# Kernel optimization log

Measured on AMD Instinct MI355X. Metric: run time of the kernel, lower is better.

The kernel has to match this reference:

```python
import jax, jax.numpy as jnp
from jax import lax
import numpy as np

N_MACRO, HIDDEN, N_LAYERS, N_REGIMES, N_ASSETS = 16, 256, 2, 3, 32
VIX_THRESHOLD, DEFENSIVE_ALLOC, EPSILON = 30.0, 0.4, 1e-8
N_EQ = 24  # equities = assets[:24], defensive = assets[24:]
N_DEF = N_ASSETS - N_EQ
LN_EPS = 1e-5


def setup_inputs() -> dict:
    key = jax.random.key(0)
    ks = jax.random.split(key, 16)
    B, S = 128, 1024
    inp = {
        'macro_features': jax.random.normal(ks[0], (B, S, N_MACRO), jnp.float32),
        'vix_values': jax.random.uniform(ks[1], (B,), jnp.float32) * 60.0,  # some above threshold
    }
    k = 1.0 / np.sqrt(HIDDEN)
    def u(kk, shape):
        return jax.random.uniform(kk, shape, jnp.float32, -k, k)
    # layer 0
    inp['lstm_Wih0'] = u(ks[2], (4 * HIDDEN, N_MACRO))
    inp['lstm_Whh0'] = u(ks[3], (4 * HIDDEN, HIDDEN))
    inp['lstm_bih0'] = u(ks[4], (4 * HIDDEN,))
    inp['lstm_bhh0'] = u(ks[5], (4 * HIDDEN,))
    # layer 1
    inp['lstm_Wih1'] = u(ks[6], (4 * HIDDEN, HIDDEN))
    inp['lstm_Whh1'] = u(ks[7], (4 * HIDDEN, HIDDEN))
    inp['lstm_bih1'] = u(ks[8], (4 * HIDDEN,))
    inp['lstm_bhh1'] = u(ks[9], (4 * HIDDEN,))
    inp['ln_gamma'] = jnp.ones((HIDDEN,), jnp.float32)
    inp['ln_beta'] = jnp.zeros((HIDDEN,), jnp.float32)
    inp['logits_W'] = u(ks[10], (N_REGIMES, HIDDEN))
    inp['logits_b'] = u(ks[11], (N_REGIMES,))
    inp['risk_budgets'] = jax.random.normal(ks[12], (N_REGIMES, N_ASSETS), jnp.float32) * 0.01
    return inp


def _lstm_layer(x, Wih, Whh, bih, bhh):
    # x: [B,S,I] -> h sequence [B,S,H]
    B = x.shape[0]
    H = Whh.shape[1]
    pre = jnp.einsum('bsi,gi->bsg', x, Wih) + bih + bhh  # [B,S,4H]
    def step(carry, p):
        h, c = carry
        g = p + h @ Whh.T
        i, f, gg, o = jnp.split(g, 4, axis=-1)
        c = jax.nn.sigmoid(f) * c + jax.nn.sigmoid(i) * jnp.tanh(gg)
        h = jax.nn.sigmoid(o) * jnp.tanh(c)
        return (h, c), h
    init = (jnp.zeros((B, H), x.dtype), jnp.zeros((B, H), x.dtype))
    _, hs = lax.scan(step, init, jnp.swapaxes(pre, 0, 1))
    return jnp.swapaxes(hs, 0, 1)


def _vix_override(beta, vix_mask):
    # vectorized version of the per-sample override loop
    eq, df = beta[:, :N_EQ], beta[:, N_EQ:]
    cur_def = df.sum(-1)
    shortfall = DEFENSIVE_ALLOC - cur_def
    eq_total = eq.sum(-1)
    ratio = jnp.minimum(shortfall / jnp.maximum(eq_total, EPSILON), 0.8)
    apply = vix_mask & (shortfall > 0) & (eq_total > EPSILON)
    new_eq = eq * (1.0 - ratio)[:, None]
    new_df = df + (shortfall / N_DEF)[:, None]
    b2 = jnp.concatenate([new_eq, new_df], axis=-1)
    b = jnp.where(apply[:, None], b2, beta)
    b_norm = b / (b.sum(-1, keepdims=True) + EPSILON)
    return jnp.where(vix_mask[:, None], b_norm, beta)


def reference(macro_features, vix_values,
              lstm_Wih0, lstm_Whh0, lstm_bih0, lstm_bhh0,
              lstm_Wih1, lstm_Whh1, lstm_bih1, lstm_bhh1,
              ln_gamma, ln_beta, logits_W, logits_b, risk_budgets):
    h1 = _lstm_layer(macro_features, lstm_Wih0, lstm_Whh0, lstm_bih0, lstm_bhh0)
    h2 = _lstm_layer(h1, lstm_Wih1, lstm_Whh1, lstm_bih1, lstm_bhh1)
    h_last = h2[:, -1, :]  # [B,H]
    mu = h_last.mean(-1, keepdims=True)
    var = ((h_last - mu) ** 2).mean(-1, keepdims=True)
    h_norm = (h_last - mu) / jnp.sqrt(var + LN_EPS) * ln_gamma + ln_beta
    regime_probs = jax.nn.softmax(h_norm @ logits_W.T + logits_b, axis=-1)  # [B,K]
    budgets = jax.nn.softmax(risk_budgets, axis=-1)  # [K,P]
    beta = jnp.einsum('bk,kp->bp', regime_probs, budgets)
    vix_mask = vix_values >= VIX_THRESHOLD
    beta = _vix_override(beta, vix_mask)
    return beta, regime_probs
```

## Files before the change

kernel.cpp:

```cpp
#include <hip/hip_runtime.h>

#define B_  128
#define S_  1024
#define H_  256
#define NM_ 16
#define NEG_INF_TGT (-0x7FFFFFFF)

typedef short bf16x8 __attribute__((ext_vector_type(8)));
typedef float f32x4  __attribute__((ext_vector_type(4)));

__device__ __forceinline__ short f2bf(float f) {
    unsigned u = __builtin_bit_cast(unsigned, f);
    unsigned r = (u + 0x7FFFu + ((u >> 16) & 1u)) >> 16;
    return (short)r;
}
__device__ __forceinline__ bf16x8 zero8() {
    bf16x8 v;
    #pragma unroll
    for (int j = 0; j < 8; ++j) v[j] = 0;
    return v;
}
__device__ __forceinline__ float sigf(float x)  { return 1.0f / (1.0f + __expf(-x)); }
__device__ __forceinline__ float tanh_(float x) { return 1.0f - 2.0f / (1.0f + __expf(2.0f * x)); }
__device__ __forceinline__ void vm_drain() {
    asm volatile("s_waitcnt vmcnt(0)" ::: "memory");
}

__device__ __forceinline__ int cload_int(const int* p) {
    int r;
    asm volatile("global_load_dword %0, %1, off sc0 sc1\n\ts_waitcnt vmcnt(0)"
                 : "=v"(r) : "v"(p) : "memory");
    return r;
}
__device__ __forceinline__ void cstore_int(int* p, int v) {
    asm volatile("global_store_dword %0, %1, off sc0 sc1" :: "v"(p), "v"(v) : "memory");
}
__device__ __forceinline__ void cstore_short(short* p, int v) {
    asm volatile("global_store_short %0, %1, off sc0 sc1" :: "v"(p), "v"(v) : "memory");
}
__device__ __forceinline__ void cload8x16(const short* p, bf16x8* d) {
    int4 a0, a1, a2, a3, a4, a5, a6, a7;
    asm volatile(
        "global_load_dwordx4 %0, %8, off sc0 sc1\n\t"
        "global_load_dwordx4 %1, %8, off offset:64 sc0 sc1\n\t"
        "global_load_dwordx4 %2, %8, off offset:128 sc0 sc1\n\t"
        "global_load_dwordx4 %3, %8, off offset:192 sc0 sc1\n\t"
        "global_load_dwordx4 %4, %8, off offset:256 sc0 sc1\n\t"
        "global_load_dwordx4 %5, %8, off offset:320 sc0 sc1\n\t"
        "global_load_dwordx4 %6, %8, off offset:384 sc0 sc1\n\t"
        "global_load_dwordx4 %7, %8, off offset:448 sc0 sc1\n\t"
        "s_waitcnt vmcnt(0)"
        : "=&v"(a0), "=&v"(a1), "=&v"(a2), "=&v"(a3),
          "=&v"(a4), "=&v"(a5), "=&v"(a6), "=&v"(a7)
        : "v"(p) : "memory");
    d[0] = __builtin_bit_cast(bf16x8, a0); d[1] = __builtin_bit_cast(bf16x8, a1);
    d[2] = __builtin_bit_cast(bf16x8, a2); d[3] = __builtin_bit_cast(bf16x8, a3);
    d[4] = __builtin_bit_cast(bf16x8, a4); d[5] = __builtin_bit_cast(bf16x8, a5);
    d[6] = __builtin_bit_cast(bf16x8, a6); d[7] = __builtin_bit_cast(bf16x8, a7);
}

__device__ __forceinline__ void tag_poll(const int* tagp, int tgt) {
    for (;;) {
        int tv = cload_int(tagp);
        if (__all(tv >= tgt)) break;
    }
}

__device__ void run_l0(const float* __restrict__ x, const float* __restrict__ Wih0,
                       const float* __restrict__ Whh0, const float* __restrict__ bih0,
                       const float* __restrict__ bhh0, short* __restrict__ h1ring,
                       int* __restrict__ tags0, int* __restrict__ tags1, int g, int q)
{
    const int lane = threadIdx.x & 63, wv = threadIdx.x >> 6;
    const int n = lane & 15, quad = lane >> 4;
    const int hu_base = q * 64 + wv * 16;
    bf16x8 wf[4][9];
    float  bias[4];
    #pragma unroll
    for (int G = 0; G < 4; ++G) {
        int col = G * 256 + hu_base + n;
        bias[G] = bih0[col] + bhh0[col];
        #pragma unroll
        for (int kt = 0; kt < 8; ++kt) {
            const float* p = Whh0 + (long)col * H_ + kt * 32 + quad * 8;
            bf16x8 v;
            #pragma unroll
            for (int j = 0; j < 8; ++j) v[j] = f2bf(p[j]);
            wf[G][kt] = v;
        }
        bf16x8 v = zero8();
        if (quad < 2) {
            const float* p = Wih0 + (long)col * NM_ + quad * 8;
            #pragma unroll
            for (int j = 0; j < 8; ++j) v[j] = f2bf(p[j]);
        }
        wf[G][8] = v;
    }
    const int bRow = g * 16 + n;
    const int* tagp = (lane < 16) ? (tags0 + (g * 16 + lane) * 16)
                    : (lane < 32) ? (tags1 + (g * 16 + lane - 16) * 16)
                                  : (tags0 + g * 16 * 16);
    int* mytag = tags0 + (g * 16 + q * 4 + wv) * 16;
    f32x4 c = {0.f, 0.f, 0.f, 0.f};
    for (int t = 0; t < S_; ++t) {
        bf16x8 xfrag = zero8();
        if (quad < 2) {
            const float* p = x + ((long)bRow * S_ + t) * NM_ + quad * 8;
            #pragma unroll
            for (int j = 0; j < 8; ++j) xfrag[j] = f2bf(p[j]);
        }
        const int tgt = (lane < 16) ? t : ((lane < 32) ? (t - 15) : NEG_INF_TGT);
        tag_poll(tagp, tgt);

        bf16x8 af[9];
        if (t > 0) {
            cload8x16(h1ring + ((long)((t - 1) & 15) * B_ + bRow) * H_ + quad * 8, af);
        } else {
            #pragma unroll
            for (int kt = 0; kt < 8; ++kt) af[kt] = zero8();
        }
        af[8] = xfrag;

        f32x4 acc[4];
        #pragma unroll
        for (int G = 0; G < 4; ++G) {
            acc[G][0] = bias[G]; acc[G][1] = bias[G];
            acc[G][2] = bias[G]; acc[G][3] = bias[G];
        }
        #pragma unroll
        for (int kt = 0; kt < 9; ++kt)
            #pragma unroll
            for (int G = 0; G < 4; ++G)
                acc[G] = __builtin_amdgcn_mfma_f32_16x16x32_bf16(af[kt], wf[G][kt], acc[G], 0, 0, 0);
        #pragma unroll
        for (int r = 0; r < 4; ++r) {
            float iv = sigf(acc[0][r]);
            float fv = sigf(acc[1][r]);
            float gv = tanh_(acc[2][r]);
            float ov = sigf(acc[3][r]);
            c[r] = fv * c[r] + iv * gv;
            float hv = ov * tanh_(c[r]);
            int b = g * 16 + quad * 4 + r;
            cstore_short(h1ring + ((long)(t & 15) * B_ + b) * H_ + hu_base + n,
                         (int)(unsigned short)f2bf(hv));
        }
        vm_drain();
        if (lane == 0) cstore_int(mytag, t + 1);
    }
}

__device__ void run_l1(const float* __restrict__ Wih1, const float* __restrict__ Whh1,
                       const float* __restrict__ bih1, const float* __restrict__ bhh1,
                       short* __restrict__ h1ring, short* __restrict__ h2ring,
                       float* __restrict__ hlast,
                       int* __restrict__ tags0, int* __restrict__ tags1, int g, int q)
{
    const int lane = threadIdx.x & 63, wv = threadIdx.x >> 6;
    const int n = lane & 15, quad = lane >> 4;
    const int hu_base = q * 64 + wv * 16;
    bf16x8 wf[4][16];
    float  bias[4];
    #pragma unroll
    for (int G = 0; G < 4; ++G) {
        int col = G * 256 + hu_base + n;
        bias[G] = bih1[col] + bhh1[col];
        #pragma unroll
        for (int kt = 0; kt < 8; ++kt) {
            const float* p = Whh1 + (long)col * H_ + kt * 32 + quad * 8;
            bf16x8 v;
            #pragma unroll
            for (int j = 0; j < 8; ++j) v[j] = f2bf(p[j]);
            wf[G][kt] = v;
        }
        #pragma unroll
        for (int kt = 0; kt < 8; ++kt) {
            const float* p = Wih1 + (long)col * H_ + kt * 32 + quad * 8;
            bf16x8 v;
            #pragma unroll
            for (int j = 0; j < 8; ++j) v[j] = f2bf(p[j]);
            wf[G][8 + kt] = v;
        }
    }
    const int bRow = g * 16 + n;
    const int* tagp = (lane < 16) ? (tags0 + (g * 16 + lane) * 16)
                    : (lane < 32) ? (tags1 + (g * 16 + lane - 16) * 16)
                                  : (tags1 + g * 16 * 16);
    int* mytag = tags1 + (g * 16 + q * 4 + wv) * 16;
    f32x4 c = {0.f, 0.f, 0.f, 0.f};
    for (int t = 0; t < S_; ++t) {
        const int tgt = (lane < 16) ? (t + 1) : ((lane < 32) ? t : NEG_INF_TGT);
        tag_poll(tagp, tgt);

        bf16x8 af[16];
        if (t > 0) {
            cload8x16(h2ring + ((long)((t - 1) & 1) * B_ + bRow) * H_ + quad * 8, af);
        } else {
            #pragma unroll
            for (int kt = 0; kt < 8; ++kt) af[kt] = zero8();
        }
        cload8x16(h1ring + ((long)(t & 15) * B_ + bRow) * H_ + quad * 8, af + 8);

        f32x4 acc[4];
        #pragma unroll
        for (int G = 0; G < 4; ++G) {
            acc[G][0] = bias[G]; acc[G][1] = bias[G];
            acc[G][2] = bias[G]; acc[G][3] = bias[G];
        }
        #pragma unroll
        for (int kt = 0; kt < 16; ++kt)
            #pragma unroll
            for (int G = 0; G < 4; ++G)
                acc[G] = __builtin_amdgcn_mfma_f32_16x16x32_bf16(af[kt], wf[G][kt], acc[G], 0, 0, 0);
        #pragma unroll
        for (int r = 0; r < 4; ++r) {
            float iv = sigf(acc[0][r]);
            float fv = sigf(acc[1][r]);
            float gv = tanh_(acc[2][r]);
            float ov = sigf(acc[3][r]);
            c[r] = fv * c[r] + iv * gv;
            float hv = ov * tanh_(c[r]);
            int b = g * 16 + quad * 4 + r;
            cstore_short(h2ring + ((long)(t & 1) * B_ + b) * H_ + hu_base + n,
                         (int)(unsigned short)f2bf(hv));
            if (t == S_ - 1) hlast[b * H_ + hu_base + n] = hv;
        }
        vm_drain();
        if (lane == 0) cstore_int(mytag, t + 1);
    }
}

__global__ __launch_bounds__(256, 1) void lstm_kernel(
    const float* __restrict__ x,
    const float* __restrict__ Wih0, const float* __restrict__ Whh0,
    const float* __restrict__ bih0, const float* __restrict__ bhh0,
    const float* __restrict__ Wih1, const float* __restrict__ Whh1,
    const float* __restrict__ bih1, const float* __restrict__ bhh1,
    short* __restrict__ h1ring, short* __restrict__ h2ring,
    float* __restrict__ hlast,
    int* __restrict__ tags0, int* __restrict__ tags1)
{
    const int g    = blockIdx.x & 7;
    const int role = blockIdx.x >> 3;
    if (role < 4) run_l0(x, Wih0, Whh0, bih0, bhh0, h1ring, tags0, tags1, g, role);
    else          run_l1(Wih1, Whh1, bih1, bhh1, h1ring, h2ring, hlast, tags0, tags1, g, role - 4);
}

__device__ __forceinline__ float blockSum(float v, float* sbuf) {
    #pragma unroll
    for (int off = 32; off > 0; off >>= 1) v += __shfl_down(v, off, 64);
    __syncthreads();
    if ((threadIdx.x & 63) == 0) sbuf[threadIdx.x >> 6] = v;
    __syncthreads();
    return sbuf[0] + sbuf[1] + sbuf[2] + sbuf[3];
}

__global__ __launch_bounds__(256) void tail_kernel(
    const float* __restrict__ hlast, const float* __restrict__ gamma,
    const float* __restrict__ lnbeta, const float* __restrict__ Wl,
    const float* __restrict__ bl, const float* __restrict__ rb,
    const float* __restrict__ vix, float* __restrict__ out)
{
    __shared__ float sbuf[4];
    __shared__ float pr[3], mxs[3], dens[3];
    __shared__ float bvec[32];
    const int b   = blockIdx.x;
    const int tid = threadIdx.x;

    float v  = hlast[b * H_ + tid];
    float mu = blockSum(v, sbuf) * (1.0f / 256.0f);
    float d  = v - mu;
    float var = blockSum(d * d, sbuf) * (1.0f / 256.0f);
    float hn  = d * rsqrtf(var + 1e-5f) * gamma[tid] + lnbeta[tid];

    float l[3];
    #pragma unroll
    for (int k = 0; k < 3; ++k)
        l[k] = blockSum(hn * Wl[k * H_ + tid], sbuf) + bl[k];

    if (tid == 0) {
        float m  = fmaxf(l[0], fmaxf(l[1], l[2]));
        float e0 = __expf(l[0] - m), e1 = __expf(l[1] - m), e2 = __expf(l[2] - m);
        float dn = e0 + e1 + e2;
        pr[0] = e0 / dn; pr[1] = e1 / dn; pr[2] = e2 / dn;
    }
    if (tid < 3) {
        float m = -1e30f;
        for (int p = 0; p < 32; ++p) m = fmaxf(m, rb[tid * 32 + p]);
        float dn = 0.f;
        for (int p = 0; p < 32; ++p) dn += __expf(rb[tid * 32 + p] - m);
        mxs[tid] = m; dens[tid] = dn;
    }
    __syncthreads();
    if (tid < 32) {
        float bp = 0.f;
        #pragma unroll
        for (int k = 0; k < 3; ++k)
            bp += pr[k] * __expf(rb[k * 32 + tid] - mxs[k]) / dens[k];
        bvec[tid] = bp;
    }
    __syncthreads();
    if (tid == 0) {
        bool  mask = vix[b] >= 30.0f;
        float eq_total = 0.f, cur_def = 0.f;
        for (int p = 0; p < 24; ++p) eq_total += bvec[p];
        for (int p = 24; p < 32; ++p) cur_def += bvec[p];
        float shortfall = 0.4f - cur_def;
        float ratio = fminf(shortfall / fmaxf(eq_total, 1e-8f), 0.8f);
        bool  apply = mask && (shortfall > 0.0f) && (eq_total > 1e-8f);
        float bb[32]; float ssum = 0.f;
        for (int p = 0; p < 32; ++p) {
            float b2 = (p < 24) ? bvec[p] * (1.0f - ratio) : bvec[p] + shortfall * (1.0f / 8.0f);
            float bv = apply ? b2 : bvec[p];
            bb[p] = bv; ssum += bv;
        }
        float inv = 1.0f / (ssum + 1e-8f);
        for (int p = 0; p < 32; ++p)
            out[b * 32 + p] = mask ? bb[p] * inv : bvec[p];
        #pragma unroll
        for (int k = 0; k < 3; ++k)
            out[B_ * 32 + b * 3 + k] = pr[k];
    }
}

extern "C" void kernel_launch(void* const* d_in, const int* in_sizes, int n_in,
                              void* d_out, int out_size, void* d_ws, size_t ws_size,
                              hipStream_t stream)
{
    const float* x    = (const float*)d_in[0];
    const float* vix  = (const float*)d_in[1];
    const float* Wih0 = (const float*)d_in[2];
    const float* Whh0 = (const float*)d_in[3];
    const float* bih0 = (const float*)d_in[4];
    const float* bhh0 = (const float*)d_in[5];
    const float* Wih1 = (const float*)d_in[6];
    const float* Whh1 = (const float*)d_in[7];
    const float* bih1 = (const float*)d_in[8];
    const float* bhh1 = (const float*)d_in[9];
    const float* lng  = (const float*)d_in[10];
    const float* lnb  = (const float*)d_in[11];
    const float* Wl   = (const float*)d_in[12];
    const float* bl   = (const float*)d_in[13];
    const float* rb   = (const float*)d_in[14];
    float* out = (float*)d_out;

    char*  ws     = (char*)d_ws;
    short* h1ring = (short*)ws;
    short* h2ring = (short*)(ws + 1048576);
    float* hlast  = (float*)(ws + 1179648);
    int*   tags0  = (int*)(ws + 1310720);
    int*   tags1  = (int*)(ws + 1318912);

    hipMemsetAsync(ws + 1310720, 0, 16384, stream);
    lstm_kernel<<<64, 256, 0, stream>>>(x, Wih0, Whh0, bih0, bhh0,
                                        Wih1, Whh1, bih1, bhh1,
                                        h1ring, h2ring, hlast, tags0, tags1);
    tail_kernel<<<128, 256, 0, stream>>>(hlast, lng, lnb, Wl, bl, rb, vix, out);
}
```

Measured before the change: 4.822 ms.

## Embed step tags in hidden-state words to replace separate flag polling

Each bf16 hidden value is stored in a 32-bit word with the low 16 bits holding the timestep tag. Consumers poll the data rows directly until every tag matches, so the separate per-wave tag stores, the drain before them, and the dependency polls are removed. Backpressure is handled with a lighter async check on layer-1 progress, and the h2 ring grows from 2 to 4 slots. In exchange the data volume moved per step doubles, and retry loops reload whole rows.

```diff
diff --git a/kernel.cpp b/kernel.cpp
--- a/kernel.cpp
+++ b/kernel.cpp
@@ -4,7 +4,6 @@
 #define S_  1024
 #define H_  256
 #define NM_ 16
-#define NEG_INF_TGT (-0x7FFFFFFF)
 
 typedef short bf16x8 __attribute__((ext_vector_type(8)));
 typedef float f32x4  __attribute__((ext_vector_type(4)));
@@ -32,44 +31,73 @@
                  : "=v"(r) : "v"(p) : "memory");
     return r;
 }
+__device__ __forceinline__ int cload_int_nw(const int* p) {
+    int r;
+    asm volatile("global_load_dword %0, %1, off sc0 sc1" : "=&v"(r) : "v"(p) : "memory");
+    return r;
+}
 __device__ __forceinline__ void cstore_int(int* p, int v) {
     asm volatile("global_store_dword %0, %1, off sc0 sc1" :: "v"(p), "v"(v) : "memory");
 }
-__device__ __forceinline__ void cstore_short(short* p, int v) {
-    asm volatile("global_store_short %0, %1, off sc0 sc1" :: "v"(p), "v"(v) : "memory");
-}
-__device__ __forceinline__ void cload8x16(const short* p, bf16x8* d) {
-    int4 a0, a1, a2, a3, a4, a5, a6, a7;
+__device__ __forceinline__ void cstore_word(unsigned* p, unsigned v) {
+    asm volatile("global_store_dword %0, %1, off sc0 sc1" :: "v"(p), "v"(v) : "memory");
+}
+__device__ __forceinline__ void row_lo_nw(const unsigned* p, int4* d) {
     asm volatile(
         "global_load_dwordx4 %0, %8, off sc0 sc1\n\t"
-        "global_load_dwordx4 %1, %8, off offset:64 sc0 sc1\n\t"
+        "global_load_dwordx4 %1, %8, off offset:16 sc0 sc1\n\t"
         "global_load_dwordx4 %2, %8, off offset:128 sc0 sc1\n\t"
-        "global_load_dwordx4 %3, %8, off offset:192 sc0 sc1\n\t"
+        "global_load_dwordx4 %3, %8, off offset:144 sc0 sc1\n\t"
         "global_load_dwordx4 %4, %8, off offset:256 sc0 sc1\n\t"
-        "global_load_dwordx4 %5, %8, off offset:320 sc0 sc1\n\t"
+        "global_load_dwordx4 %5, %8, off offset:272 sc0 sc1\n\t"
         "global_load_dwordx4 %6, %8, off offset:384 sc0 sc1\n\t"
-        "global_load_dwordx4 %7, %8, off offset:448 sc0 sc1\n\t"
-        "s_waitcnt vmcnt(0)"
-        : "=&v"(a0), "=&v"(a1), "=&v"(a2), "=&v"(a3),
-          "=&v"(a4), "=&v"(a5), "=&v"(a6), "=&v"(a7)
+        "global_load_dwordx4 %7, %8, off offset:400 sc0 sc1"
+        : "=&v"(d[0]), "=&v"(d[1]), "=&v"(d[2]), "=&v"(d[3]),
+          "=&v"(d[4]), "=&v"(d[5]), "=&v"(d[6]), "=&v"(d[7])
         : "v"(p) : "memory");
-    d[0] = __builtin_bit_cast(bf16x8, a0); d[1] = __builtin_bit_cast(bf16x8, a1);
-    d[2] = __builtin_bit_cast(bf16x8, a2); d[3] = __builtin_bit_cast(bf16x8, a3);
-    d[4] = __builtin_bit_cast(bf16x8, a4); d[5] = __builtin_bit_cast(bf16x8, a5);
-    d[6] = __builtin_bit_cast(bf16x8, a6); d[7] = __builtin_bit_cast(bf16x8, a7);
-}
-
-__device__ __forceinline__ void tag_poll(const int* tagp, int tgt) {
-    for (;;) {
-        int tv = cload_int(tagp);
-        if (__all(tv >= tgt)) break;
+}
+__device__ __forceinline__ void row_hi_nw(const unsigned* p, int4* d) {
+    asm volatile(
+        "global_load_dwordx4 %0, %8, off offset:512 sc0 sc1\n\t"
+        "global_load_dwordx4 %1, %8, off offset:528 sc0 sc1\n\t"
+        "global_load_dwordx4 %2, %8, off offset:640 sc0 sc1\n\t"
+        "global_load_dwordx4 %3, %8, off offset:656 sc0 sc1\n\t"
+        "global_load_dwordx4 %4, %8, off offset:768 sc0 sc1\n\t"
+        "global_load_dwordx4 %5, %8, off offset:784 sc0 sc1\n\t"
+        "global_load_dwordx4 %6, %8, off offset:896 sc0 sc1\n\t"
+        "global_load_dwordx4 %7, %8, off offset:912 sc0 sc1"
+        : "=&v"(d[0]), "=&v"(d[1]), "=&v"(d[2]), "=&v"(d[3]),
+          "=&v"(d[4]), "=&v"(d[5]), "=&v"(d[6]), "=&v"(d[7])
+        : "v"(p) : "memory");
+}
+__device__ __forceinline__ unsigned tagmask16(const int4* w, unsigned tgt) {
+    unsigned mm = 0;
+    #pragma unroll
+    for (int i = 0; i < 16; ++i) {
+        mm |= ((unsigned)w[i].x ^ tgt) & 0xFFFFu;
+        mm |= ((unsigned)w[i].y ^ tgt) & 0xFFFFu;
+        mm |= ((unsigned)w[i].z ^ tgt) & 0xFFFFu;
+        mm |= ((unsigned)w[i].w ^ tgt) & 0xFFFFu;
+    }
+    return mm;
+}
+__device__ __forceinline__ void unpack8(const int4* w, bf16x8* af) {
+    #pragma unroll
+    for (int k = 0; k < 8; ++k) {
+        int4 A = w[2 * k], Bv = w[2 * k + 1];
+        int4 r;
+        r.x = (int)(((unsigned)A.x  >> 16) | ((unsigned)A.y  & 0xFFFF0000u));
+        r.y = (int)(((unsigned)A.z  >> 16) | ((unsigned)A.w  & 0xFFFF0000u));
+        r.z = (int)(((unsigned)Bv.x >> 16) | ((unsigned)Bv.y & 0xFFFF0000u));
+        r.w = (int)(((unsigned)Bv.z >> 16) | ((unsigned)Bv.w & 0xFFFF0000u));
+        af[k] = __builtin_bit_cast(bf16x8, r);
     }
 }
 
 __device__ void run_l0(const float* __restrict__ x, const float* __restrict__ Wih0,
                        const float* __restrict__ Whh0, const float* __restrict__ bih0,
-                       const float* __restrict__ bhh0, short* __restrict__ h1ring,
-                       int* __restrict__ tags0, int* __restrict__ tags1, int g, int q)
+                       const float* __restrict__ bhh0, unsigned* __restrict__ h1w,
+                       int* __restrict__ tags1, int g, int q)
 {
     const int lane = threadIdx.x & 63, wv = threadIdx.x >> 6;
     const int n = lane & 15, quad = lane >> 4;
@@ -96,11 +124,9 @@
         }
         wf[G][8] = v;
     }
-    const int bRow = g * 16 + n;
-    const int* tagp = (lane < 16) ? (tags0 + (g * 16 + lane) * 16)
-                    : (lane < 32) ? (tags1 + (g * 16 + lane - 16) * 16)
-                                  : (tags0 + g * 16 * 16);
-    int* mytag = tags0 + (g * 16 + q * 4 + wv) * 16;
+    const int  bRow = g * 16 + n;
+    const bool bplane = (lane >= 16 && lane < 32);
+    const int* tp = tags1 + (g * 16 + ((lane - 16) & 15)) * 16;
     f32x4 c = {0.f, 0.f, 0.f, 0.f};
     for (int t = 0; t < S_; ++t) {
         bf16x8 xfrag = zero8();
@@ -109,17 +135,29 @@
             #pragma unroll
             for (int j = 0; j < 8; ++j) xfrag[j] = f2bf(p[j]);
         }
-        const int tgt = (lane < 16) ? t : ((lane < 32) ? (t - 15) : NEG_INF_TGT);
-        tag_poll(tagp, tgt);
-
         bf16x8 af[9];
         if (t > 0) {
-            cload8x16(h1ring + ((long)((t - 1) & 15) * B_ + bRow) * H_ + quad * 8, af);
+            const unsigned tgt = (unsigned)t & 0xFFFFu;
+            const unsigned* p = h1w + ((long)((t - 1) & 15) * B_ + bRow) * H_ + quad * 8;
+            int4 raw[16];
+            row_lo_nw(p, raw); row_hi_nw(p, raw + 8);
+            vm_drain(); __builtin_amdgcn_sched_barrier(0);
+            for (;;) {
+                unsigned mm = tagmask16(raw, tgt);
+                if (__all(mm == 0)) break;
+                __builtin_amdgcn_s_sleep(1);
+                row_lo_nw(p, raw); row_hi_nw(p, raw + 8);
+                vm_drain(); __builtin_amdgcn_sched_barrier(0);
+            }
+            unpack8(raw, af);
         } else {
             #pragma unroll
             for (int kt = 0; kt < 8; ++kt) af[kt] = zero8();
         }
         af[8] = xfrag;
+
+        int bpv = 0;
+        if (bplane) bpv = cload_int_nw(tp);
 
         f32x4 acc[4];
         #pragma unroll
@@ -132,6 +170,8 @@
             #pragma unroll
             for (int G = 0; G < 4; ++G)
                 acc[G] = __builtin_amdgcn_mfma_f32_16x16x32_bf16(af[kt], wf[G][kt], acc[G], 0, 0, 0);
+
+        unsigned wd[4];
         #pragma unroll
         for (int r = 0; r < 4; ++r) {
             float iv = sigf(acc[0][r]);
@@ -140,20 +180,29 @@
             float ov = sigf(acc[3][r]);
             c[r] = fv * c[r] + iv * gv;
             float hv = ov * tanh_(c[r]);
+            wd[r] = ((unsigned)(unsigned short)f2bf(hv) << 16) | ((unsigned)(t + 1) & 0xFFFFu);
+        }
+        vm_drain(); __builtin_amdgcn_sched_barrier(0);
+        {
+            const int bptgt = t - 15;
+            int ok = bplane ? (bpv >= bptgt) : 1;
+            while (!__all(ok)) {
+                if (bplane) bpv = cload_int(tp);
+                ok = bplane ? (bpv >= bptgt) : 1;
+            }
+        }
+        #pragma unroll
+        for (int r = 0; r < 4; ++r) {
             int b = g * 16 + quad * 4 + r;
-            cstore_short(h1ring + ((long)(t & 15) * B_ + b) * H_ + hu_base + n,
-                         (int)(unsigned short)f2bf(hv));
-        }
-        vm_drain();
-        if (lane == 0) cstore_int(mytag, t + 1);
+            cstore_word(h1w + ((long)(t & 15) * B_ + b) * H_ + hu_base + n, wd[r]);
+        }
     }
 }
 
 __device__ void run_l1(const float* __restrict__ Wih1, const float* __restrict__ Whh1,
                        const float* __restrict__ bih1, const float* __restrict__ bhh1,
-                       short* __restrict__ h1ring, short* __restrict__ h2ring,
-                       float* __restrict__ hlast,
-                       int* __restrict__ tags0, int* __restrict__ tags1, int g, int q)
+                       unsigned* __restrict__ h1w, unsigned* __restrict__ h2w,
+                       float* __restrict__ hlast, int* __restrict__ tags1, int g, int q)
 {
     const int lane = threadIdx.x & 63, wv = threadIdx.x >> 6;
     const int n = lane & 15, quad = lane >> 4;
@@ -181,24 +230,42 @@
             wf[G][8 + kt] = v;
         }
     }
-    const int bRow = g * 16 + n;
-    const int* tagp = (lane < 16) ? (tags0 + (g * 16 + lane) * 16)
-                    : (lane < 32) ? (tags1 + (g * 16 + lane - 16) * 16)
-                                  : (tags1 + g * 16 * 16);
+    const int  bRow = g * 16 + n;
+    const bool bplane = (lane >= 16 && lane < 32);
+    const int* tp = tags1 + (g * 16 + ((lane - 16) & 15)) * 16;
     int* mytag = tags1 + (g * 16 + q * 4 + wv) * 16;
     f32x4 c = {0.f, 0.f, 0.f, 0.f};
     for (int t = 0; t < S_; ++t) {
-        const int tgt = (lane < 16) ? (t + 1) : ((lane < 32) ? t : NEG_INF_TGT);
-        tag_poll(tagp, tgt);
+        const unsigned tgt2 = (unsigned)t & 0xFFFFu;
+        const unsigned tgt1 = (unsigned)(t + 1) & 0xFFFFu;
+        const unsigned* p2 = h2w + ((long)((t - 1) & 3) * B_ + bRow) * H_ + quad * 8;
+        const unsigned* p1 = h1w + ((long)(t & 15) * B_ + bRow) * H_ + quad * 8;
+        int4 raw2[16], raw1[16];
+        if (t > 0) { row_lo_nw(p2, raw2); row_hi_nw(p2, raw2 + 8); }
+        row_lo_nw(p1, raw1); row_hi_nw(p1, raw1 + 8);
+        vm_drain(); __builtin_amdgcn_sched_barrier(0);
+        for (;;) {
+            unsigned mm = tagmask16(raw1, tgt1);
+            if (t > 0) mm |= tagmask16(raw2, tgt2);
+            if (__all(mm == 0)) break;
+            __builtin_amdgcn_s_sleep(1);
+            if (t > 0) { row_lo_nw(p2, raw2); row_hi_nw(p2, raw2 + 8); }
+            row_lo_nw(p1, raw1); row_hi_nw(p1, raw1 + 8);
+            vm_drain(); __builtin_amdgcn_sched_barrier(0);
+        }
+        if (lane == 0) cstore_int(mytag, t + 1);
+
+        int bpv = 0;
+        if (bplane) bpv = cload_int_nw(tp);
 
         bf16x8 af[16];
         if (t > 0) {
-            cload8x16(h2ring + ((long)((t - 1) & 1) * B_ + bRow) * H_ + quad * 8, af);
+            unpack8(raw2, af);
         } else {
             #pragma unroll
             for (int kt = 0; kt < 8; ++kt) af[kt] = zero8();
         }
-        cload8x16(h1ring + ((long)(t & 15) * B_ + bRow) * H_ + quad * 8, af + 8);
+        unpack8(raw1, af + 8);
 
         f32x4 acc[4];
         #pragma unroll
@@ -211,6 +278,8 @@
             #pragma unroll
             for (int G = 0; G < 4; ++G)
                 acc[G] = __builtin_amdgcn_mfma_f32_16x16x32_bf16(af[kt], wf[G][kt], acc[G], 0, 0, 0);
+
+        unsigned wd[4]; float hvout[4];
         #pragma unroll
         for (int r = 0; r < 4; ++r) {
             float iv = sigf(acc[0][r]);
@@ -219,13 +288,24 @@
             float ov = sigf(acc[3][r]);
             c[r] = fv * c[r] + iv * gv;
             float hv = ov * tanh_(c[r]);
+            hvout[r] = hv;
+            wd[r] = ((unsigned)(unsigned short)f2bf(hv) << 16) | ((unsigned)(t + 1) & 0xFFFFu);
+        }
+        vm_drain(); __builtin_amdgcn_sched_barrier(0);
+        {
+            const int bptgt = t - 2;
+            int ok = bplane ? (bpv >= bptgt) : 1;
+            while (!__all(ok)) {
+                if (bplane) bpv = cload_int(tp);
+                ok = bplane ? (bpv >= bptgt) : 1;
+            }
+        }
+        #pragma unroll
+        for (int r = 0; r < 4; ++r) {
             int b = g * 16 + quad * 4 + r;
-            cstore_short(h2ring + ((long)(t & 1) * B_ + b) * H_ + hu_base + n,
-                         (int)(unsigned short)f2bf(hv));
-            if (t == S_ - 1) hlast[b * H_ + hu_base + n] = hv;
-        }
-        vm_drain();
-        if (lane == 0) cstore_int(mytag, t + 1);
+            cstore_word(h2w + ((long)(t & 3) * B_ + b) * H_ + hu_base + n, wd[r]);
+            if (t == S_ - 1) hlast[b * H_ + hu_base + n] = hvout[r];
+        }
     }
 }
 
@@ -235,14 +315,13 @@
     const float* __restrict__ bih0, const float* __restrict__ bhh0,
     const float* __restrict__ Wih1, const float* __restrict__ Whh1,
     const float* __restrict__ bih1, const float* __restrict__ bhh1,
-    short* __restrict__ h1ring, short* __restrict__ h2ring,
-    float* __restrict__ hlast,
-    int* __restrict__ tags0, int* __restrict__ tags1)
+    unsigned* __restrict__ h1w, unsigned* __restrict__ h2w,
+    float* __restrict__ hlast, int* __restrict__ tags1)
 {
     const int g    = blockIdx.x & 7;
     const int role = blockIdx.x >> 3;
-    if (role < 4) run_l0(x, Wih0, Whh0, bih0, bhh0, h1ring, tags0, tags1, g, role);
-    else          run_l1(Wih1, Whh1, bih1, bhh1, h1ring, h2ring, hlast, tags0, tags1, g, role - 4);
+    if (role < 4) run_l0(x, Wih0, Whh0, bih0, bhh0, h1w, tags1, g, role);
+    else          run_l1(Wih1, Whh1, bih1, bhh1, h1w, h2w, hlast, tags1, g, role - 4);
 }
 
 __device__ __forceinline__ float blockSum(float v, float* sbuf) {
@@ -343,16 +422,16 @@
     const float* rb   = (const float*)d_in[14];
     float* out = (float*)d_out;
 
-    char*  ws     = (char*)d_ws;
-    short* h1ring = (short*)ws;
-    short* h2ring = (short*)(ws + 1048576);
-    float* hlast  = (float*)(ws + 1179648);
-    int*   tags0  = (int*)(ws + 1310720);
-    int*   tags1  = (int*)(ws + 1318912);
-
-    hipMemsetAsync(ws + 1310720, 0, 16384, stream);
+    char*     ws    = (char*)d_ws;
+    unsigned* h1w   = (unsigned*)ws;
+    unsigned* h2w   = (unsigned*)(ws + 2097152);
+    float*    hlast = (float*)(ws + 2621440);
+    int*      tags1 = (int*)(ws + 2752512);
+
+    (void)hipMemsetAsync(ws, 0, 2621440, stream);
+    (void)hipMemsetAsync(ws + 2752512, 0, 8192, stream);
     lstm_kernel<<<64, 256, 0, stream>>>(x, Wih0, Whh0, bih0, bhh0,
                                         Wih1, Whh1, bih1, bhh1,
-                                        h1ring, h2ring, hlast, tags0, tags1);
+                                        h1w, h2w, hlast, tags1);
     tail_kernel<<<128, 256, 0, stream>>>(hlast, lng, lnb, Wl, bl, rb, vix, out);
 }
```

After: 9.850 ms. +104.3%, slower.
